# Kernel tuning notes

Hardware: AMD Instinct MI355X
Metric: run time of the kernel (lower is better)

## Reference

```python
import jax, jax.numpy as jnp
import numpy as np

B, T, I, E, K, J = 4, 4096, 1024, 16, 512, 1024

def setup_inputs() -> dict:
    key = jax.random.key(0)
    k1, k2, k3 = jax.random.split(key, 3)
    X = jax.random.normal(k1, (B, T, I), dtype=jnp.float32)
    ind = jax.random.randint(k2, (B, E, K), 0, T, dtype=jnp.int64)
    W = jax.random.normal(k3, (E, I, J), dtype=jnp.float32)
    return {"X": X, "ind": ind, "W": W}

def reference(X, ind, W):
    b, t, i = X.shape
    # offset each batch's indices into the flattened [B*T, I] token table
    offset = jnp.arange(b, dtype=ind.dtype)[:, None, None] * t  # [B,1,1]
    X_flat = X.reshape(b * t, i)
    X_gathered = X_flat[ind + offset]  # [B,E,K,I] irregular gather
    Y = jnp.einsum('beki,eij->bekj', X_gathered, W)  # grouped GEMM per expert
    return Y
```

## Files before the change

### kernel.cpp

```cpp
#include <hip/hip_runtime.h>

#define DI __device__ __forceinline__

constexpr int Bc = 4, Tc = 4096, Ic = 1024, Ec = 16, Kc = 512, Jc = 1024;

typedef __attribute__((ext_vector_type(8))) short short8;
typedef __attribute__((ext_vector_type(4))) float floatx4;

DI unsigned pack2_bf16(float a, float b) {
  union { float f; unsigned u; } ua, ub;
  ua.f = a; ub.f = b;
  const unsigned x = ua.u + 0x8000u;
  const unsigned y = ub.u + 0x8000u;
#if __has_builtin(__builtin_amdgcn_perm)
  return __builtin_amdgcn_perm(y, x, 0x07060302u);
#else
  return (x >> 16) | (y & 0xFFFF0000u);
#endif
}

DI void async_load16(const void* g, void* lds) {
  __builtin_amdgcn_global_load_lds((const __attribute__((address_space(1))) void*)g,
                                   (__attribute__((address_space(3))) void*)lds,
                                   16, 0, 0);
}

__global__ __launch_bounds__(256) void prep(const float* __restrict__ X,
                                            const int* __restrict__ ind,
                                            const float* __restrict__ W,
                                            unsigned short* __restrict__ Xg,
                                            unsigned short* __restrict__ Wt) {
  __shared__ __align__(16) char smem[32 * 260 * 2];
  const int bid = blockIdx.x >> 1;
  const int t = threadIdx.x;

  if ((blockIdx.x & 1) == 0) {
    unsigned short* Ls = (unsigned short*)smem;
    const int g = t >> 5, kk = t & 31;
    const int R = bid * 8 + g;
    const int b = R >> 13;
    const int xr = ind[R];
    const float* src = X + ((size_t)(b * Tc + xr)) * Ic + kk * 32;
    unsigned u[16];
#pragma unroll
    for (int q = 0; q < 8; ++q) {
      const float4 v = *(const float4*)(src + q * 4);
      u[2 * q]     = pack2_bf16(v.x, v.y);
      u[2 * q + 1] = pack2_bf16(v.z, v.w);
    }
    unsigned short* lp = &Ls[kk * 260 + g * 32];
#pragma unroll
    for (int q = 0; q < 4; ++q) *(uint4*)(lp + q * 8) = *(uint4*)&u[4 * q];
    __syncthreads();
    const int kk2 = t >> 3, rw = t & 7;
    const int tt = bid >> 4;
    const int rl0 = (bid & 15) * 8;
    unsigned short* dst = Xg + ((size_t)(tt * 32 + kk2) * 128 + rl0 + rw) * 32;
    const unsigned short* lr = &Ls[kk2 * 260 + rw * 32];
#pragma unroll
    for (int q = 0; q < 4; ++q) *(uint4*)(dst + q * 8) = *(const uint4*)(lr + q * 8);
  } else {
    float (*tile)[129] = (float(*)[129])smem;
    const int kk = bid & 31;
    const int jt = (bid >> 5) & 7;
    const int e  = bid >> 8;
    const float* Wp = W + ((size_t)(e * Ic + kk * 32)) * Jc + jt * 128;
#pragma unroll
    for (int p = 0; p < 4; ++p) {
      const int il = p * 8 + (t >> 5);
      const int c4 = (t & 31) * 4;
      const float4 v = *(const float4*)(Wp + (size_t)il * Jc + c4);
      tile[il][c4 + 0] = v.x; tile[il][c4 + 1] = v.y;
      tile[il][c4 + 2] = v.z; tile[il][c4 + 3] = v.w;
    }
    __syncthreads();
    unsigned short* out = Wt + ((size_t)((e * 8 + jt) * 32 + kk)) * 4096;
#pragma unroll
    for (int h = 0; h < 2; ++h) {
      const int n   = h * 64 + (t >> 2);
      const int il0 = (t & 3) * 8;
      unsigned u[4];
#pragma unroll
      for (int q = 0; q < 4; ++q)
        u[q] = pack2_bf16(tile[il0 + 2 * q][n], tile[il0 + 2 * q + 1][n]);
      *(uint4*)(out + (size_t)(h * 256 + t) * 8) = *(uint4*)u;
    }
  }
}

__global__ __launch_bounds__(256) void moe_gemm(const unsigned short* __restrict__ Xg,
                                                const unsigned short* __restrict__ Wt,
                                                float* __restrict__ Y) {
  __shared__ unsigned short As[2 * 128 * 32];
  __shared__ unsigned short Bs[2 * 128 * 32];

  const int bid = blockIdx.x;
  const int jt = bid >> 8;
  const int rr = bid & 255;
  const int b  = rr >> 6;
  const int e  = (rr >> 2) & 15;
  const int kt = rr & 3;

  const int t = threadIdx.x;
  const int w = t >> 6;
  const int l = t & 63;
  const int nl  = l >> 2;
  const int csw = (l & 3) ^ (nl & 3);

  const int atile = (b * Ec + e) * 4 + kt;
  const unsigned short* abase = Xg + (size_t)atile * 32 * 4096;
  const unsigned short* bbase = Wt + (size_t)((e * 8 + jt) * 32) * 4096;

  int loff[2];
  unsigned short *adst[2], *bdst[2];
#pragma unroll
  for (int p = 0; p < 2; ++p) {
    const int rg = w * 2 + p;
    loff[p] = (rg * 16 + nl) * 32 + csw * 8;
    adst[p] = &As[rg * 512];
    bdst[p] = &Bs[rg * 512];
  }

  floatx4 acc[4][4];
#pragma unroll
  for (int tm = 0; tm < 4; ++tm)
#pragma unroll
    for (int tn = 0; tn < 4; ++tn) acc[tm][tn] = (floatx4){0.f, 0.f, 0.f, 0.f};

  const int wm = (w & 1) * 64;
  const int wn = (w >> 1) * 64;
  const int lrow = l & 15;
  const int quad = l >> 4;
  const int swz  = lrow & 3;

  for (int kk2 = 0; kk2 < 16; ++kk2) {
    __syncthreads();
#pragma unroll
    for (int s = 0; s < 2; ++s) {
      const size_t cb = (size_t)(kk2 * 2 + s) * 4096;
#pragma unroll
      for (int p = 0; p < 2; ++p) {
        async_load16(abase + cb + loff[p], adst[p] + s * 4096);
        async_load16(bbase + cb + loff[p], bdst[p] + s * 4096);
      }
    }
    __syncthreads();

#pragma unroll
    for (int s = 0; s < 2; ++s) {
      short8 af[4], bf[4];
#pragma unroll
      for (int tm = 0; tm < 4; ++tm)
        af[tm] = *(const short8*)&As[s * 4096 + (wm + tm * 16 + lrow) * 32 + (quad ^ swz) * 8];
#pragma unroll
      for (int tn = 0; tn < 4; ++tn)
        bf[tn] = *(const short8*)&Bs[s * 4096 + (wn + tn * 16 + lrow) * 32 + (quad ^ swz) * 8];
#pragma unroll
      for (int tm = 0; tm < 4; ++tm)
#pragma unroll
        for (int tn = 0; tn < 4; ++tn)
          acc[tm][tn] = __builtin_amdgcn_mfma_f32_16x16x32_bf16(af[tm], bf[tn], acc[tm][tn], 0, 0, 0);
    }
  }

  float* Yp = Y + ((size_t)(b * Ec + e) * Kc + (size_t)kt * 128) * Jc + jt * 128;
#pragma unroll
  for (int tm = 0; tm < 4; ++tm) {
#pragma unroll
    for (int tn = 0; tn < 4; ++tn) {
#pragma unroll
      for (int r = 0; r < 4; ++r) {
        const int row = wm + tm * 16 + quad * 4 + r;
        const int col = wn + tn * 16 + lrow;
        Yp[(size_t)row * Jc + col] = acc[tm][tn][r];
      }
    }
  }
}

extern "C" void kernel_launch(void* const* d_in, const int* in_sizes, int n_in,
                              void* d_out, int out_size, void* d_ws, size_t ws_size,
                              hipStream_t stream) {
  const float* X = (const float*)d_in[0];
  const int* ind = (const int*)d_in[1];
  const float* W = (const float*)d_in[2];
  float* Y = (float*)d_out;

  unsigned short* Xg = (unsigned short*)d_ws;
  unsigned short* Wt = (unsigned short*)d_ws + (size_t)Bc * Ec * Kc * Ic;

  hipLaunchKernelGGL(prep, dim3(8192), dim3(256), 0, stream, X, ind, W, Xg, Wt);
  hipLaunchKernelGGL(moe_gemm, dim3(Bc * Ec * 4 * 8), dim3(256), 0, stream, Xg, Wt, Y);
}
```

Measured before the change: 347.8 us.

## Rewrite grouped GEMM with 256x256 tiles and a four-stage async LDS pipeline

The GEMM kernel moves from 128x128 tiles with 256 threads to 256x256 tiles with 512 threads, so each wave holds an 8x4 grid of MFMA accumulators. Global-to-LDS loads now go through a four-buffer ring issued three steps ahead. Explicit vmcnt waits plus a single barrier per k-step replace the two __syncthreads around every load, so loads overlap with MFMA work. It also adds an XOR swizzle on the LDS layout, a block-index remap that groups tiles of the same expert, and s_setprio around the MFMA bursts. In exchange it raises register and LDS pressure and shrinks the grid to 512 blocks, which risks lower occupancy and a poorer wave-count balance across CUs.

```diff
diff --git a/kernel.cpp b/kernel.cpp
--- a/kernel.cpp
+++ b/kernel.cpp
@@ -88,90 +88,107 @@
   }
 }
 
-__global__ __launch_bounds__(256) void moe_gemm(const unsigned short* __restrict__ Xg,
-                                                const unsigned short* __restrict__ Wt,
-                                                float* __restrict__ Y) {
-  __shared__ unsigned short As[2 * 128 * 32];
-  __shared__ unsigned short Bs[2 * 128 * 32];
-
-  const int bid = blockIdx.x;
-  const int jt = bid >> 8;
-  const int rr = bid & 255;
-  const int b  = rr >> 6;
-  const int e  = (rr >> 2) & 15;
-  const int kt = rr & 3;
+__global__ __launch_bounds__(512, 2) void moe_gemm(const unsigned short* __restrict__ Xg,
+                                                   const unsigned short* __restrict__ Wt,
+                                                   float* __restrict__ Y) {
+  __shared__ __align__(16) unsigned short As[4 * 8192];
+  __shared__ __align__(16) unsigned short Bs[4 * 8192];
+
+  const int bid   = blockIdx.x;
+  const int lg    = (bid & 7) * 64 + (bid >> 3);
+  const int e     = lg >> 5;
+  const int inner = lg & 31;
+  const int b     = inner >> 3;
+  const int mt    = (inner >> 2) & 1;
+  const int nt    = inner & 3;
 
   const int t = threadIdx.x;
   const int w = t >> 6;
   const int l = t & 63;
-  const int nl  = l >> 2;
-  const int csw = (l & 3) ^ (nl & 3);
-
-  const int atile = (b * Ec + e) * 4 + kt;
-  const unsigned short* abase = Xg + (size_t)atile * 32 * 4096;
-  const unsigned short* bbase = Wt + (size_t)((e * 8 + jt) * 32) * 4096;
-
-  int loff[2];
-  unsigned short *adst[2], *bdst[2];
-#pragma unroll
-  for (int p = 0; p < 2; ++p) {
-    const int rg = w * 2 + p;
-    loff[p] = (rg * 16 + nl) * 32 + csw * 8;
-    adst[p] = &As[rg * 512];
-    bdst[p] = &Bs[rg * 512];
+  const int lrow = l & 15;
+  const int q    = l >> 4;
+
+  const int tt0 = b * 64 + e * 4 + mt * 2;
+  const int jg0 = e * 8 + nt * 2;
+
+  const int sr = t >> 2, sc = t & 3;
+  const size_t lsrc = (size_t)sr * 32 + ((sc ^ ((sr >> 1) & 3)) << 3);
+
+  const unsigned short* aC = Xg + (size_t)tt0 * 32 * 4096 + lsrc;
+  const unsigned short* bC = Wt + (size_t)jg0 * 32 * 4096 + lsrc;
+  unsigned short* aL = As + w * 512;
+  unsigned short* bL = Bs + w * 512;
+
+  auto stage = [&](int k3) {
+    const int bu = (k3 & 3) * 8192;
+#pragma unroll
+    for (int p = 0; p < 2; ++p) {
+      async_load16(aC + ((size_t)(p * 32 + k3)) * 4096, aL + bu + p * 4096);
+      async_load16(bC + ((size_t)(p * 32 + k3)) * 4096, bL + bu + p * 4096);
+    }
+  };
+
+  floatx4 acc[8][4];
+#pragma unroll
+  for (int tm = 0; tm < 8; ++tm)
+#pragma unroll
+    for (int tn = 0; tn < 4; ++tn) acc[tm][tn] = (floatx4){0.f, 0.f, 0.f, 0.f};
+
+  const int pos = (q ^ ((lrow >> 1) & 3)) << 3;
+  const unsigned short* Ard = As + ((w >> 2) << 12) + lrow * 32 + pos;
+  const unsigned short* Brd = Bs + (((w >> 1) & 1) << 12) + ((w & 1) * 64 + lrow) * 32 + pos;
+
+  stage(0); stage(1); stage(2);
+
+  auto compute = [&](int kt) {
+    const int bu = (kt & 3) * 8192;
+    short8 bf[4];
+#pragma unroll
+    for (int tn = 0; tn < 4; ++tn) bf[tn] = *(const short8*)(Brd + bu + tn * 512);
+    __builtin_amdgcn_s_setprio(1);
+#pragma unroll
+    for (int h = 0; h < 2; ++h) {
+      short8 af[4];
+#pragma unroll
+      for (int i2 = 0; i2 < 4; ++i2)
+        af[i2] = *(const short8*)(Ard + bu + (h * 4 + i2) * 512);
+#pragma unroll
+      for (int i2 = 0; i2 < 4; ++i2)
+#pragma unroll
+        for (int tn = 0; tn < 4; ++tn)
+          acc[h * 4 + i2][tn] =
+              __builtin_amdgcn_mfma_f32_16x16x32_bf16(af[i2], bf[tn], acc[h * 4 + i2][tn], 0, 0, 0);
+    }
+    __builtin_amdgcn_s_setprio(0);
+  };
+
+#define WAITVM(n) asm volatile("s_waitcnt vmcnt(" #n ")" ::: "memory")
+#define CFENCE    asm volatile("" ::: "memory")
+
+#pragma unroll 4
+  for (int kt = 0; kt < 28; ++kt) {
+    WAITVM(8);
+    __builtin_amdgcn_s_barrier();
+    CFENCE;
+    stage(kt + 3);
+    compute(kt);
   }
-
-  floatx4 acc[4][4];
-#pragma unroll
-  for (int tm = 0; tm < 4; ++tm)
-#pragma unroll
-    for (int tn = 0; tn < 4; ++tn) acc[tm][tn] = (floatx4){0.f, 0.f, 0.f, 0.f};
-
-  const int wm = (w & 1) * 64;
-  const int wn = (w >> 1) * 64;
-  const int lrow = l & 15;
-  const int quad = l >> 4;
-  const int swz  = lrow & 3;
-
-  for (int kk2 = 0; kk2 < 16; ++kk2) {
-    __syncthreads();
-#pragma unroll
-    for (int s = 0; s < 2; ++s) {
-      const size_t cb = (size_t)(kk2 * 2 + s) * 4096;
-#pragma unroll
-      for (int p = 0; p < 2; ++p) {
-        async_load16(abase + cb + loff[p], adst[p] + s * 4096);
-        async_load16(bbase + cb + loff[p], bdst[p] + s * 4096);
-      }
-    }
-    __syncthreads();
-
-#pragma unroll
-    for (int s = 0; s < 2; ++s) {
-      short8 af[4], bf[4];
-#pragma unroll
-      for (int tm = 0; tm < 4; ++tm)
-        af[tm] = *(const short8*)&As[s * 4096 + (wm + tm * 16 + lrow) * 32 + (quad ^ swz) * 8];
-#pragma unroll
-      for (int tn = 0; tn < 4; ++tn)
-        bf[tn] = *(const short8*)&Bs[s * 4096 + (wn + tn * 16 + lrow) * 32 + (quad ^ swz) * 8];
-#pragma unroll
-      for (int tm = 0; tm < 4; ++tm)
-#pragma unroll
-        for (int tn = 0; tn < 4; ++tn)
-          acc[tm][tn] = __builtin_amdgcn_mfma_f32_16x16x32_bf16(af[tm], bf[tn], acc[tm][tn], 0, 0, 0);
-    }
-  }
-
-  float* Yp = Y + ((size_t)(b * Ec + e) * Kc + (size_t)kt * 128) * Jc + jt * 128;
-#pragma unroll
-  for (int tm = 0; tm < 4; ++tm) {
+  WAITVM(8); __builtin_amdgcn_s_barrier(); CFENCE; stage(31); compute(28);
+  WAITVM(8); __builtin_amdgcn_s_barrier(); CFENCE; compute(29);
+  WAITVM(4); __builtin_amdgcn_s_barrier(); CFENCE; compute(30);
+  WAITVM(0); __builtin_amdgcn_s_barrier(); CFENCE; compute(31);
+
+  float* Yp = Y + (((size_t)(b * Ec + e) * Kc + (size_t)mt * 256) * Jc) + nt * 256;
+  const int wmRow = (w >> 2) * 128;
+  const int wnCol = (w & 3) * 64;
+#pragma unroll
+  for (int tm = 0; tm < 8; ++tm) {
 #pragma unroll
     for (int tn = 0; tn < 4; ++tn) {
 #pragma unroll
       for (int r = 0; r < 4; ++r) {
-        const int row = wm + tm * 16 + quad * 4 + r;
-        const int col = wn + tn * 16 + lrow;
+        const int row = wmRow + tm * 16 + q * 4 + r;
+        const int col = wnCol + tn * 16 + lrow;
         Yp[(size_t)row * Jc + col] = acc[tm][tn][r];
       }
     }
@@ -190,5 +207,5 @@
   unsigned short* Wt = (unsigned short*)d_ws + (size_t)Bc * Ec * Kc * Ic;
 
   hipLaunchKernelGGL(prep, dim3(8192), dim3(256), 0, stream, X, ind, W, Xg, Wt);
-  hipLaunchKernelGGL(moe_gemm, dim3(Bc * Ec * 4 * 8), dim3(256), 0, stream, Xg, Wt, Y);
-}
+  hipLaunchKernelGGL(moe_gemm, dim3(512), dim3(512), 0, stream, Xg, Wt, Y);
+}
```

Measured after the change: 327.7 us. 1.06x faster.
